# Kernel tuning notes

Measured on AMD Instinct MI355X. Metric: run time of the kernel, lower is better.

The kernel has to match this reference:

```python
import jax, jax.numpy as jnp
import numpy as np

LN_EPS = 1e-5


def setup_inputs() -> dict:
    key = jax.random.key(0)
    k_x, k_w, k_g, k_b = jax.random.split(key, 4)
    P, N, C_IN, C_OUT = 62, 8192, 128, 256
    x = jax.random.normal(k_x, (P, N, C_IN), dtype=jnp.float32)
    # per-part Linear(in, out, bias=False) weights, torch layout [out, in]
    W = jax.random.normal(k_w, (P, C_OUT, C_IN), dtype=jnp.float32) * (1.0 / np.sqrt(C_IN))
    # final LayerNorm affine params (after_norm_type='LN', affine=True)
    gamma = jnp.ones((C_OUT,), dtype=jnp.float32)
    beta = jnp.zeros((C_OUT,), dtype=jnp.float32)
    return {"x": x, "W": W, "gamma": gamma, "beta": beta}


def _layer_norm(h, gamma, beta):
    mu = jnp.mean(h, axis=-1, keepdims=True)
    var = jnp.mean(jnp.square(h - mu), axis=-1, keepdims=True)
    return (h - mu) * jax.lax.rsqrt(var + LN_EPS) * gamma + beta


def reference(x, W, gamma, beta):
    # pre_norm='None' and mid_norm='None' are identities; the per-part Python
    # loop of Linear layers is a single batched GEMM over the part dim.
    # x: [P, N, C_in], W: [P, C_out, C_in] -> h: [P, N, C_out]
    h = jnp.einsum('pnc,pdc->pnd', x, W)
    # final LayerNorm applied over the channel dim (view(-1, d) is equivalent)
    return _layer_norm(h, gamma, beta)
```

## Files before the change

kernel.cpp:

```cpp
#include <hip/hip_runtime.h>
#include <cstdint>
#include <cstddef>

typedef __bf16  bf16x8  __attribute__((ext_vector_type(8)));
typedef short   shortx8 __attribute__((ext_vector_type(8)));
typedef float   f32x4   __attribute__((ext_vector_type(4)));

constexpr int P_PARTS     = 62;
constexpr int N_TOK       = 8192;
constexpr int C_IN        = 128;
constexpr int C_OUT       = 256;
constexpr int ROWS_PER_WG = 512;
constexpr int ROWS_ITER   = 64;
constexpr int N_ITER      = ROWS_PER_WG / ROWS_ITER;
constexpr int WG_PER_PART = N_TOK / ROWS_PER_WG;
constexpr int XSTRIDE     = C_IN + 8;
constexpr float LN_EPS    = 1e-5f;

__device__ __forceinline__ short f2bf_rne(float f) {
    uint32_t u = __float_as_uint(f);
    u += 0x7FFFu + ((u >> 16) & 1u);
    return (short)(u >> 16);
}

union FragU { shortx8 s; bf16x8 b; };

__device__ __forceinline__ bf16x8 cvt8(f32x4 a, f32x4 b) {
    FragU fu;
    fu.s[0] = f2bf_rne(a[0]); fu.s[1] = f2bf_rne(a[1]);
    fu.s[2] = f2bf_rne(a[2]); fu.s[3] = f2bf_rne(a[3]);
    fu.s[4] = f2bf_rne(b[0]); fu.s[5] = f2bf_rne(b[1]);
    fu.s[6] = f2bf_rne(b[2]); fu.s[7] = f2bf_rne(b[3]);
    return fu.b;
}

extern "C" __global__ void __launch_bounds__(256, 3)
fused_fc_ln(const float* __restrict__ x, const float* __restrict__ Wt,
            const float* __restrict__ gamma, const float* __restrict__ beta,
            float* __restrict__ out)
{
    __shared__ __align__(16) short xs[ROWS_ITER * XSTRIDE];
    __shared__ float psum[ROWS_ITER][4];
    __shared__ float psq [ROWS_ITER][4];
    __shared__ float rmean[ROWS_ITER];
    __shared__ float rrstd[ROWS_ITER];

    const int tid  = threadIdx.x;
    const int wv   = tid >> 6;
    const int lane = tid & 63;
    const int quad = lane >> 4;
    const int l16  = lane & 15;

    const int part = blockIdx.x >> 4;
    const int rb   = blockIdx.x & 15;
    const long rowBase = (long)part * N_TOK + (long)rb * ROWS_PER_WG;

    bf16x8 bfrag[4][4];
    float g[4], bt[4];
    #pragma unroll
    for (int ct = 0; ct < 4; ++ct) {
        const int d = wv * 64 + ct * 16 + l16;
        g[ct]  = gamma[d];
        bt[ct] = beta[d];
        const float* wp = Wt + ((size_t)part * C_OUT + d) * C_IN + quad * 8;
        #pragma unroll
        for (int kk = 0; kk < 4; ++kk) {
            const f32x4* p4 = (const f32x4*)(wp + kk * 32);
            bfrag[ct][kk] = cvt8(p4[0], p4[1]);
        }
    }

    const float* xblk = x   + rowBase * C_IN;
    float*       oblk = out + rowBase * C_OUT;

    for (int it = 0; it < N_ITER; ++it) {
        const float* xsrc = xblk + (size_t)it * (ROWS_ITER * C_IN);
        #pragma unroll
        for (int i = 0; i < 4; ++i) {
            const int c  = tid + i * 256;
            const int r  = c >> 4;
            const int ck = c & 15;
            const f32x4* p4 = (const f32x4*)(xsrc + (size_t)c * 8);
            FragU fu; fu.b = cvt8(p4[0], p4[1]);
            *(shortx8*)&xs[r * XSTRIDE + ck * 8] = fu.s;
        }
        __syncthreads();

        f32x4 acc[4][4];
        #pragma unroll
        for (int rt = 0; rt < 4; ++rt)
            #pragma unroll
            for (int ct = 0; ct < 4; ++ct)
                acc[rt][ct] = f32x4{0.f, 0.f, 0.f, 0.f};

        #pragma unroll
        for (int rt = 0; rt < 4; ++rt) {
            const int row = rt * 16 + l16;
            bf16x8 af[4];
            #pragma unroll
            for (int kk = 0; kk < 4; ++kk)
                af[kk] = *(const bf16x8*)&xs[row * XSTRIDE + (kk * 4 + quad) * 8];
            #pragma unroll
            for (int ct = 0; ct < 4; ++ct)
                #pragma unroll
                for (int kk = 0; kk < 4; ++kk)
                    acc[rt][ct] = __builtin_amdgcn_mfma_f32_16x16x32_bf16(
                        af[kk], bfrag[ct][kk], acc[rt][ct], 0, 0, 0);
        }

        #pragma unroll
        for (int rt = 0; rt < 4; ++rt) {
            #pragma unroll
            for (int rg = 0; rg < 4; ++rg) {
                float a0 = acc[rt][0][rg], a1 = acc[rt][1][rg];
                float a2 = acc[rt][2][rg], a3 = acc[rt][3][rg];
                float s  = a0 + a1 + a2 + a3;
                float s2 = a0*a0 + a1*a1 + a2*a2 + a3*a3;
                #pragma unroll
                for (int off = 1; off < 16; off <<= 1) {
                    s  += __shfl_xor(s,  off, 64);
                    s2 += __shfl_xor(s2, off, 64);
                }
                if (l16 == 0) {
                    const int row = rt * 16 + quad * 4 + rg;
                    psum[row][wv] = s;
                    psq [row][wv] = s2;
                }
            }
        }
        __syncthreads();

        if (tid < ROWS_ITER) {
            const float s   = psum[tid][0] + psum[tid][1] + psum[tid][2] + psum[tid][3];
            const float q   = psq [tid][0] + psq [tid][1] + psq [tid][2] + psq [tid][3];
            const float mu  = s * (1.0f / C_OUT);
            const float var = q * (1.0f / C_OUT) - mu * mu;
            rmean[tid] = mu;
            rrstd[tid] = rsqrtf(var + LN_EPS);
        }
        __syncthreads();

        float* od = oblk + (size_t)it * (ROWS_ITER * C_OUT);
        #pragma unroll
        for (int rt = 0; rt < 4; ++rt) {
            #pragma unroll
            for (int rg = 0; rg < 4; ++rg) {
                const int row = rt * 16 + quad * 4 + rg;
                const float mu = rmean[row];
                const float rs = rrstd[row];
                float* orow = od + (size_t)row * C_OUT + wv * 64 + l16;
                #pragma unroll
                for (int ct = 0; ct < 4; ++ct)
                    orow[ct * 16] = (acc[rt][ct][rg] - mu) * rs * g[ct] + bt[ct];
            }
        }
    }
}

extern "C" void kernel_launch(void* const* d_in, const int* in_sizes, int n_in,
                              void* d_out, int out_size, void* d_ws, size_t ws_size,
                              hipStream_t stream) {
    const float* x     = (const float*)d_in[0];
    const float* Wt    = (const float*)d_in[1];
    const float* gamma = (const float*)d_in[2];
    const float* beta  = (const float*)d_in[3];
    float* out = (float*)d_out;
    (void)in_sizes; (void)n_in; (void)d_ws; (void)ws_size; (void)out_size;
    fused_fc_ln<<<dim3(P_PARTS * WG_PER_PART), dim3(256), 0, stream>>>(
        x, Wt, gamma, beta, out);
}
```

Baseline: 742.3 us.

## Load x fragments directly from global, drop LDS staging and a barrier

Each wave now loads its A fragments straight from global memory and converts them in registers, so the shared-memory staging buffer for x and its barrier are gone. The per-row LayerNorm statistics are finished redundantly by every thread from double-buffered partial sums, which removes a second barrier. The change also uses DPP row-rotate reductions in place of shuffles, nontemporal output stores, hardware bf16 conversion and a remapped block index that spreads parts across XCDs. The cost is that each of the four waves reads the same x rows from global/L2 memory instead of sharing one copy.

```diff
diff --git a/kernel.cpp b/kernel.cpp
--- a/kernel.cpp
+++ b/kernel.cpp
@@ -3,7 +3,6 @@
 #include <cstddef>
 
 typedef __bf16  bf16x8  __attribute__((ext_vector_type(8)));
-typedef short   shortx8 __attribute__((ext_vector_type(8)));
 typedef float   f32x4   __attribute__((ext_vector_type(4)));
 
 constexpr int P_PARTS     = 62;
@@ -14,24 +13,30 @@
 constexpr int ROWS_ITER   = 64;
 constexpr int N_ITER      = ROWS_PER_WG / ROWS_ITER;
 constexpr int WG_PER_PART = N_TOK / ROWS_PER_WG;
-constexpr int XSTRIDE     = C_IN + 8;
+constexpr int NWG         = P_PARTS * WG_PER_PART;
 constexpr float LN_EPS    = 1e-5f;
 
-__device__ __forceinline__ short f2bf_rne(float f) {
-    uint32_t u = __float_as_uint(f);
-    u += 0x7FFFu + ((u >> 16) & 1u);
-    return (short)(u >> 16);
+__device__ __forceinline__ bf16x8 cvt8(f32x4 a, f32x4 b) {
+    bf16x8 r;
+    #pragma unroll
+    for (int j = 0; j < 4; ++j) {
+        r[j]     = (__bf16)a[j];
+        r[j + 4] = (__bf16)b[j];
+    }
+    return r;
 }
 
-union FragU { shortx8 s; bf16x8 b; };
-
-__device__ __forceinline__ bf16x8 cvt8(f32x4 a, f32x4 b) {
-    FragU fu;
-    fu.s[0] = f2bf_rne(a[0]); fu.s[1] = f2bf_rne(a[1]);
-    fu.s[2] = f2bf_rne(a[2]); fu.s[3] = f2bf_rne(a[3]);
-    fu.s[4] = f2bf_rne(b[0]); fu.s[5] = f2bf_rne(b[1]);
-    fu.s[6] = f2bf_rne(b[2]); fu.s[7] = f2bf_rne(b[3]);
-    return fu.b;
+template <int CTRL>
+__device__ __forceinline__ float ror16_add(float s) {
+    int t = __builtin_amdgcn_update_dpp(0, __float_as_int(s), CTRL, 0xf, 0xf, false);
+    return s + __int_as_float(t);
+}
+__device__ __forceinline__ float red16(float s) {
+    s = ror16_add<0x128>(s);
+    s = ror16_add<0x124>(s);
+    s = ror16_add<0x122>(s);
+    s = ror16_add<0x121>(s);
+    return s;
 }
 
 extern "C" __global__ void __launch_bounds__(256, 3)
@@ -39,11 +44,8 @@
             const float* __restrict__ gamma, const float* __restrict__ beta,
             float* __restrict__ out)
 {
-    __shared__ __align__(16) short xs[ROWS_ITER * XSTRIDE];
-    __shared__ float psum[ROWS_ITER][4];
-    __shared__ float psq [ROWS_ITER][4];
-    __shared__ float rmean[ROWS_ITER];
-    __shared__ float rrstd[ROWS_ITER];
+    __shared__ __align__(16) float psum[2][ROWS_ITER][4];
+    __shared__ __align__(16) float psq [2][ROWS_ITER][4];
 
     const int tid  = threadIdx.x;
     const int wv   = tid >> 6;
@@ -51,8 +53,9 @@
     const int quad = lane >> 4;
     const int l16  = lane & 15;
 
-    const int part = blockIdx.x >> 4;
-    const int rb   = blockIdx.x & 15;
+    const int wg   = (blockIdx.x & 7) * (NWG / 8) + (blockIdx.x >> 3);
+    const int part = wg >> 4;
+    const int rb   = wg & 15;
     const long rowBase = (long)part * N_TOK + (long)rb * ROWS_PER_WG;
 
     bf16x8 bfrag[4][4];
@@ -72,19 +75,10 @@
 
     const float* xblk = x   + rowBase * C_IN;
     float*       oblk = out + rowBase * C_OUT;
+    const float  invC = 1.0f / C_OUT;
 
     for (int it = 0; it < N_ITER; ++it) {
-        const float* xsrc = xblk + (size_t)it * (ROWS_ITER * C_IN);
-        #pragma unroll
-        for (int i = 0; i < 4; ++i) {
-            const int c  = tid + i * 256;
-            const int r  = c >> 4;
-            const int ck = c & 15;
-            const f32x4* p4 = (const f32x4*)(xsrc + (size_t)c * 8);
-            FragU fu; fu.b = cvt8(p4[0], p4[1]);
-            *(shortx8*)&xs[r * XSTRIDE + ck * 8] = fu.s;
-        }
-        __syncthreads();
+        const float* xt = xblk + (size_t)it * (ROWS_ITER * C_IN);
 
         f32x4 acc[4][4];
         #pragma unroll
@@ -95,48 +89,41 @@
 
         #pragma unroll
         for (int rt = 0; rt < 4; ++rt) {
-            const int row = rt * 16 + l16;
-            bf16x8 af[4];
+            const float* xr = xt + (size_t)(rt * 16 + l16) * C_IN + quad * 8;
+            f32x4 lo[4], hi[4];
             #pragma unroll
-            for (int kk = 0; kk < 4; ++kk)
-                af[kk] = *(const bf16x8*)&xs[row * XSTRIDE + (kk * 4 + quad) * 8];
+            for (int kk = 0; kk < 4; ++kk) {
+                const f32x4* p = (const f32x4*)(xr + kk * 32);
+                lo[kk] = p[0];
+                hi[kk] = p[1];
+            }
             #pragma unroll
-            for (int ct = 0; ct < 4; ++ct)
+            for (int kk = 0; kk < 4; ++kk) {
+                const bf16x8 af = cvt8(lo[kk], hi[kk]);
                 #pragma unroll
-                for (int kk = 0; kk < 4; ++kk)
+                for (int ct = 0; ct < 4; ++ct)
                     acc[rt][ct] = __builtin_amdgcn_mfma_f32_16x16x32_bf16(
-                        af[kk], bfrag[ct][kk], acc[rt][ct], 0, 0, 0);
+                        af, bfrag[ct][kk], acc[rt][ct], 0, 0, 0);
+            }
         }
 
+        const int sb = it & 1;
         #pragma unroll
         for (int rt = 0; rt < 4; ++rt) {
             #pragma unroll
             for (int rg = 0; rg < 4; ++rg) {
-                float a0 = acc[rt][0][rg], a1 = acc[rt][1][rg];
-                float a2 = acc[rt][2][rg], a3 = acc[rt][3][rg];
-                float s  = a0 + a1 + a2 + a3;
-                float s2 = a0*a0 + a1*a1 + a2*a2 + a3*a3;
-                #pragma unroll
-                for (int off = 1; off < 16; off <<= 1) {
-                    s  += __shfl_xor(s,  off, 64);
-                    s2 += __shfl_xor(s2, off, 64);
-                }
+                const float a0 = acc[rt][0][rg], a1 = acc[rt][1][rg];
+                const float a2 = acc[rt][2][rg], a3 = acc[rt][3][rg];
+                float s  = (a0 + a1) + (a2 + a3);
+                float s2 = (a0 * a0 + a1 * a1) + (a2 * a2 + a3 * a3);
+                s  = red16(s);
+                s2 = red16(s2);
                 if (l16 == 0) {
                     const int row = rt * 16 + quad * 4 + rg;
-                    psum[row][wv] = s;
-                    psq [row][wv] = s2;
+                    psum[sb][row][wv] = s;
+                    psq [sb][row][wv] = s2;
                 }
             }
-        }
-        __syncthreads();
-
-        if (tid < ROWS_ITER) {
-            const float s   = psum[tid][0] + psum[tid][1] + psum[tid][2] + psum[tid][3];
-            const float q   = psq [tid][0] + psq [tid][1] + psq [tid][2] + psq [tid][3];
-            const float mu  = s * (1.0f / C_OUT);
-            const float var = q * (1.0f / C_OUT) - mu * mu;
-            rmean[tid] = mu;
-            rrstd[tid] = rsqrtf(var + LN_EPS);
         }
         __syncthreads();
 
@@ -146,12 +133,18 @@
             #pragma unroll
             for (int rg = 0; rg < 4; ++rg) {
                 const int row = rt * 16 + quad * 4 + rg;
-                const float mu = rmean[row];
-                const float rs = rrstd[row];
+                const f32x4 ps = *(const f32x4*)&psum[sb][row][0];
+                const f32x4 pq = *(const f32x4*)&psq [sb][row][0];
+                const float s  = (ps[0] + ps[1]) + (ps[2] + ps[3]);
+                const float q  = (pq[0] + pq[1]) + (pq[2] + pq[3]);
+                const float mu = s * invC;
+                const float rs = rsqrtf(q * invC - mu * mu + LN_EPS);
                 float* orow = od + (size_t)row * C_OUT + wv * 64 + l16;
                 #pragma unroll
                 for (int ct = 0; ct < 4; ++ct)
-                    orow[ct * 16] = (acc[rt][ct][rg] - mu) * rs * g[ct] + bt[ct];
+                    __builtin_nontemporal_store(
+                        (acc[rt][ct][rg] - mu) * rs * g[ct] + bt[ct],
+                        orow + ct * 16);
             }
         }
     }
@@ -166,6 +159,5 @@
     const float* beta  = (const float*)d_in[3];
     float* out = (float*)d_out;
     (void)in_sizes; (void)n_in; (void)d_ws; (void)ws_size; (void)out_size;
-    fused_fc_ln<<<dim3(P_PARTS * WG_PER_PART), dim3(256), 0, stream>>>(
-        x, Wt, gamma, beta, out);
+    fused_fc_ln<<<dim3(NWG), dim3(256), 0, stream>>>(x, Wt, gamma, beta, out);
 }
```

Result: slower. 829.1 us (+11.7%).
